# Kernel optimization log

Measured on AMD Instinct MI355X. Metric: run time of the kernel, lower is better.

The kernel has to match this reference:

```python
import jax, jax.numpy as jnp
import numpy as np


def setup_inputs() -> dict:
    key = jax.random.key(0)
    ks = jax.random.split(key, 6)
    B, S, D, E = 4, 8192, 2048, 8
    scale = 1.0 / np.sqrt(D)
    return {
        "x": jax.random.normal(ks[0], (B, S, D), dtype=jnp.float32),
        "Wg": jax.random.normal(ks[1], (E, D), dtype=jnp.float32) * scale,
        "bg": jax.random.normal(ks[2], (E,), dtype=jnp.float32) * scale,
        "Wn": jax.random.normal(ks[3], (E, D), dtype=jnp.float32) * scale,
        "bn": jax.random.normal(ks[4], (E,), dtype=jnp.float32) * scale,
        "noise": jax.random.normal(ks[5], (B, S, E), dtype=jnp.float32),
        "k": 2,
    }


def reference(x, Wg, bg, Wn, bn, noise, k):
    # gate and noisy-gate projections: [B,S,D] x [E,D] -> [B,S,E]
    gate_logits = jnp.einsum("bsd,ed->bse", x, Wg) + bg
    noisy_pre = jnp.einsum("bsd,ed->bse", x, Wn) + bn
    noisy_logits = noise * jax.nn.softplus(noisy_pre) + gate_logits

    # top-k over experts (largest, sorted), matching torch.topk
    topklogits, topexperts = jax.lax.top_k(noisy_logits, k)  # [B,S,k]

    # softmax over sparse logits (-inf elsewhere) == softmax over the topk
    # values, scattered back; small E,k so a one-hot scatter is cheap.
    topk_probs = jax.nn.softmax(topklogits, axis=-1)          # [B,S,k]
    onehot = jax.nn.one_hot(topexperts, noisy_logits.shape[-1],
                            dtype=topk_probs.dtype)           # [B,S,k,E]
    router_output = jnp.einsum("bsk,bske->bse", topk_probs, onehot)
    return router_output, topexperts
```

## Files before the change

kernel.cpp:

```cpp
#include <hip/hip_runtime.h>
#include <math.h>


#define RD 2048
#define RE 8
#define NE16 16
#define TOKB 64
#define CH 32
#define KSL 2
#define KLEN (RD / KSL)
#define NCH (KLEN / CH)
#define NW 4
#define DEPTH 4

#define AS1 __attribute__((address_space(1)))
#define AS3 __attribute__((address_space(3)))

#define WAITVM(N) asm volatile("s_waitcnt vmcnt(" #N ")" ::: "memory")

__device__ __forceinline__ void gload_lds16(const float* g, float* l) {
    __builtin_amdgcn_global_load_lds((const AS1 unsigned int*)g,
                                     (AS3 unsigned int*)l, 16, 0, 0);
}

__global__ __launch_bounds__(256) void transpose_w_kernel(
    const float* __restrict__ Wg, const float* __restrict__ Wn,
    float* __restrict__ WT)
{
    const int idx = blockIdx.x * 256 + threadIdx.x;
    const int d = idx >> 4;
    const int e = idx & 15;
    WT[idx] = (e < 8) ? Wg[e * RD + d] : Wn[(e - 8) * RD + d];
}

__global__ __launch_bounds__(256) void router_main_kernel(
    const float* __restrict__ x,
    const float* __restrict__ WT,
    float* __restrict__ pws,
    int T)
{
    __shared__ float xb[DEPTH][TOKB * CH];

    const int tid = threadIdx.x;
    const int w = tid >> 6;
    const int l = tid & 63;
    const int NTB = T / TOKB;
    const int bt = blockIdx.x % NTB;
    const int kslice = blockIdx.x / NTB;
    const int tokBase = bt * TOKB;
    const int kbase = kslice * KLEN;

    float acc[NE16];
#pragma unroll
    for (int e = 0; e < NE16; ++e) acc[e] = 0.f;

    const size_t laneoff = (size_t)(l >> 3) * RD + ((((l & 7) ^ (l >> 3))) << 2);
    const float* p0 = x + (size_t)(tokBase + (w * 2 + 0) * 8) * RD + kbase + laneoff;
    const float* p1 = x + (size_t)(tokBase + (w * 2 + 1) * 8) * RD + kbase + laneoff;
    float* d0base = &xb[0][(w * 2 + 0) * 256];
    float* d1base = &xb[0][(w * 2 + 1) * 256];

    gload_lds16(p0 + 0 * CH, d0base + 0 * (TOKB * CH));
    gload_lds16(p1 + 0 * CH, d1base + 0 * (TOKB * CH));
    gload_lds16(p0 + 1 * CH, d0base + 1 * (TOKB * CH));
    gload_lds16(p1 + 1 * CH, d1base + 1 * (TOKB * CH));

#pragma unroll 1
    for (int c = 0; c < NCH; ++c) {
        const int b = c & (DEPTH - 1);

        if (c + 2 < NCH) {
            const int nb = (c + 2) & (DEPTH - 1);
            gload_lds16(p0 + (c + 2) * CH, d0base + nb * (TOKB * CH));
            gload_lds16(p1 + (c + 2) * CH, d1base + nb * (TOKB * CH));
            WAITVM(4);
        } else if (c + 2 == NCH) {
            WAITVM(2);
        } else {
            WAITVM(0);
        }
        __builtin_amdgcn_s_barrier();
        __builtin_amdgcn_sched_barrier(0);

        const int wbase = __builtin_amdgcn_readfirstlane(
            (kbase + c * CH + w * 8) * NE16);
        const float* __restrict__ wt = WT + wbase;
#pragma unroll
        for (int r = 0; r < 2; ++r) {
            const int q = w * 2 + r;
            const float4 xq = *reinterpret_cast<const float4*>(
                &xb[b][l * CH + ((q ^ (l & 7)) << 2)]);
            const float xs[4] = {xq.x, xq.y, xq.z, xq.w};
#pragma unroll
            for (int ii = 0; ii < 4; ++ii) {
                const float* wrow = wt + (r * 4 + ii) * NE16;
#pragma unroll
                for (int e = 0; e < NE16; ++e)
                    acc[e] = fmaf(xs[ii], wrow[e], acc[e]);
            }
        }
    }

    __syncthreads();

    float* red = &xb[0][0];
    {
        const int roff = (w * TOKB + l) * NE16;
        *reinterpret_cast<float4*>(&red[roff + 0])  = make_float4(acc[0], acc[1], acc[2], acc[3]);
        *reinterpret_cast<float4*>(&red[roff + 4])  = make_float4(acc[4], acc[5], acc[6], acc[7]);
        *reinterpret_cast<float4*>(&red[roff + 8])  = make_float4(acc[8], acc[9], acc[10], acc[11]);
        *reinterpret_cast<float4*>(&red[roff + 12]) = make_float4(acc[12], acc[13], acc[14], acc[15]);
    }
    __syncthreads();

    {
        const int tok = tid >> 2;
        const int q4 = tid & 3;
        float4 s = make_float4(0.f, 0.f, 0.f, 0.f);
#pragma unroll
        for (int wv = 0; wv < NW; ++wv) {
            const float4 a = *reinterpret_cast<const float4*>(
                &red[(wv * TOKB + tok) * NE16 + q4 * 4]);
            s.x += a.x; s.y += a.y; s.z += a.z; s.w += a.w;
        }
        float* dst = pws + ((size_t)kslice * T + tokBase + tok) * NE16 + q4 * 4;
        *reinterpret_cast<float4*>(dst) = s;
    }
}

__global__ __launch_bounds__(256) void router_finalize_kernel(
    const float* __restrict__ pws,
    const float* __restrict__ bg,
    const float* __restrict__ bn,
    const float* __restrict__ noise,
    float* __restrict__ out_router,
    float* __restrict__ out_experts,
    int T)
{
    const int tok = blockIdx.x * 256 + threadIdx.x;

    const float* pp0 = pws + (size_t)tok * NE16;
    const float* pp1 = pws + ((size_t)T + tok) * NE16;

    float g[RE], nn[RE];
#pragma unroll
    for (int e = 0; e < RE; ++e) {
        g[e]  = pp0[e] + pp1[e] + bg[e];
        nn[e] = pp0[8 + e] + pp1[8 + e] + bn[e];
    }

    const float4* nzp = reinterpret_cast<const float4*>(noise + (size_t)tok * RE);
    const float4 nz0 = nzp[0];
    const float4 nz1 = nzp[1];
    const float nzv[RE] = {nz0.x, nz0.y, nz0.z, nz0.w,
                           nz1.x, nz1.y, nz1.z, nz1.w};

    float v[RE];
#pragma unroll
    for (int e = 0; e < RE; ++e) {
        const float p = nn[e];
        const float sp = fmaxf(p, 0.f) + log1pf(expf(-fabsf(p)));
        v[e] = fmaf(nzv[e], sp, g[e]);
    }

    int i1 = 0; float m1 = v[0];
#pragma unroll
    for (int e = 1; e < RE; ++e)
        if (v[e] > m1) { m1 = v[e]; i1 = e; }
    int i2 = -1; float m2 = -INFINITY;
#pragma unroll
    for (int e = 0; e < RE; ++e)
        if (e != i1 && v[e] > m2) { m2 = v[e]; i2 = e; }

    const float e2 = expf(m2 - m1);
    const float inv = 1.f / (1.f + e2);
    const float p1s = inv;
    const float p2s = e2 * inv;

    float r[RE];
#pragma unroll
    for (int e = 0; e < RE; ++e)
        r[e] = (e == i1) ? p1s : ((e == i2) ? p2s : 0.f);

    float4* orow = reinterpret_cast<float4*>(out_router + (size_t)tok * RE);
    orow[0] = make_float4(r[0], r[1], r[2], r[3]);
    orow[1] = make_float4(r[4], r[5], r[6], r[7]);

    float2* erow = reinterpret_cast<float2*>(out_experts + (size_t)tok * 2);
    *erow = make_float2((float)i1, (float)i2);
}

extern "C" void kernel_launch(void* const* d_in, const int* in_sizes, int n_in,
                              void* d_out, int out_size, void* d_ws, size_t ws_size,
                              hipStream_t stream) {
    const float* x   = (const float*)d_in[0];
    const float* Wg  = (const float*)d_in[1];
    const float* bg  = (const float*)d_in[2];
    const float* Wn  = (const float*)d_in[3];
    const float* bn  = (const float*)d_in[4];
    const float* nz  = (const float*)d_in[5];
    const int T = in_sizes[0] / RD;

    float* WT  = (float*)d_ws;
    float* pws = WT + (size_t)RD * NE16;

    float* out_router  = (float*)d_out;
    float* out_experts = out_router + (size_t)T * RE;

    hipLaunchKernelGGL(transpose_w_kernel, dim3((RD * NE16) / 256), dim3(256),
                       0, stream, Wg, Wn, WT);

    const int NTB = T / TOKB;
    hipLaunchKernelGGL(router_main_kernel, dim3(NTB * KSL), dim3(256), 0,
                       stream, x, WT, pws, T);

    hipLaunchKernelGGL(router_finalize_kernel, dim3(T / 256), dim3(256), 0,
                       stream, pws, bg, bn, nz, out_router, out_experts, T);
}
```

Before: 60.77 us.

## Fuse weight transpose, projection and finalize into one kernel with last-block reduction

```diff
diff --git a/kernel.cpp b/kernel.cpp
--- a/kernel.cpp
+++ b/kernel.cpp
@@ -11,7 +11,8 @@
 #define KLEN (RD / KSL)
 #define NCH (KLEN / CH)
 #define NW 4
-#define DEPTH 4
+#define DEPTH 5
+#define CHF (TOKB * CH)
 
 #define AS1 __attribute__((address_space(1)))
 #define AS3 __attribute__((address_space(3)))
@@ -23,23 +24,20 @@
                                      (AS3 unsigned int*)l, 16, 0, 0);
 }
 
-__global__ __launch_bounds__(256) void transpose_w_kernel(
-    const float* __restrict__ Wg, const float* __restrict__ Wn,
-    float* __restrict__ WT)
-{
-    const int idx = blockIdx.x * 256 + threadIdx.x;
-    const int d = idx >> 4;
-    const int e = idx & 15;
-    WT[idx] = (e < 8) ? Wg[e * RD + d] : Wn[(e - 8) * RD + d];
-}
-
-__global__ __launch_bounds__(256) void router_main_kernel(
+__global__ __launch_bounds__(256) void router_fused_kernel(
     const float* __restrict__ x,
-    const float* __restrict__ WT,
+    const float* __restrict__ Wg,
+    const float* __restrict__ bg,
+    const float* __restrict__ Wn,
+    const float* __restrict__ bn,
+    const float* __restrict__ noise,
     float* __restrict__ pws,
+    int* __restrict__ flags,
+    float* __restrict__ out_router,
+    float* __restrict__ out_experts,
     int T)
 {
-    __shared__ float xb[DEPTH][TOKB * CH];
+    __shared__ float xb[DEPTH][CHF];
 
     const int tid = threadIdx.x;
     const int w = tid >> 6;
@@ -57,48 +55,57 @@
     const size_t laneoff = (size_t)(l >> 3) * RD + ((((l & 7) ^ (l >> 3))) << 2);
     const float* p0 = x + (size_t)(tokBase + (w * 2 + 0) * 8) * RD + kbase + laneoff;
     const float* p1 = x + (size_t)(tokBase + (w * 2 + 1) * 8) * RD + kbase + laneoff;
-    float* d0base = &xb[0][(w * 2 + 0) * 256];
-    float* d1base = &xb[0][(w * 2 + 1) * 256];
-
-    gload_lds16(p0 + 0 * CH, d0base + 0 * (TOKB * CH));
-    gload_lds16(p1 + 0 * CH, d1base + 0 * (TOKB * CH));
-    gload_lds16(p0 + 1 * CH, d0base + 1 * (TOKB * CH));
-    gload_lds16(p1 + 1 * CH, d1base + 1 * (TOKB * CH));
+    float* d0 = &xb[0][(w * 2 + 0) * 256];
+    float* d1 = &xb[0][(w * 2 + 1) * 256];
+
+    gload_lds16(p0 + 0 * CH, d0 + 0 * CHF);
+    gload_lds16(p1 + 0 * CH, d1 + 0 * CHF);
+    gload_lds16(p0 + 1 * CH, d0 + 1 * CHF);
+    gload_lds16(p1 + 1 * CH, d1 + 1 * CHF);
+    gload_lds16(p0 + 2 * CH, d0 + 2 * CHF);
+    gload_lds16(p1 + 2 * CH, d1 + 2 * CHF);
+
+    int cb = 0;
+    int rb = 3;
 
 #pragma unroll 1
     for (int c = 0; c < NCH; ++c) {
-        const int b = c & (DEPTH - 1);
-
-        if (c + 2 < NCH) {
-            const int nb = (c + 2) & (DEPTH - 1);
-            gload_lds16(p0 + (c + 2) * CH, d0base + nb * (TOKB * CH));
-            gload_lds16(p1 + (c + 2) * CH, d1base + nb * (TOKB * CH));
-            WAITVM(4);
-        } else if (c + 2 == NCH) {
-            WAITVM(2);
-        } else {
-            WAITVM(0);
-        }
+        if (c <= NCH - 3)      { WAITVM(4); }
+        else if (c == NCH - 2) { WAITVM(2); }
+        else                   { WAITVM(0); }
         __builtin_amdgcn_s_barrier();
         __builtin_amdgcn_sched_barrier(0);
 
-        const int wbase = __builtin_amdgcn_readfirstlane(
-            (kbase + c * CH + w * 8) * NE16);
-        const float* __restrict__ wt = WT + wbase;
+        const int woff = __builtin_amdgcn_readfirstlane(kbase + c * CH + w * 8);
+        const float* __restrict__ wgb = Wg + woff;
+        const float* __restrict__ wnb = Wn + woff;
 #pragma unroll
         for (int r = 0; r < 2; ++r) {
             const int q = w * 2 + r;
             const float4 xq = *reinterpret_cast<const float4*>(
-                &xb[b][l * CH + ((q ^ (l & 7)) << 2)]);
+                &xb[cb][l * CH + ((q ^ (l & 7)) << 2)]);
             const float xs[4] = {xq.x, xq.y, xq.z, xq.w};
 #pragma unroll
-            for (int ii = 0; ii < 4; ++ii) {
-                const float* wrow = wt + (r * 4 + ii) * NE16;
-#pragma unroll
-                for (int e = 0; e < NE16; ++e)
-                    acc[e] = fmaf(xs[ii], wrow[e], acc[e]);
+            for (int e = 0; e < RE; ++e) {
+                const float4 a = *reinterpret_cast<const float4*>(wgb + e * RD + r * 4);
+                const float4 b = *reinterpret_cast<const float4*>(wnb + e * RD + r * 4);
+                acc[e]     = fmaf(xs[0], a.x, acc[e]);
+                acc[e]     = fmaf(xs[1], a.y, acc[e]);
+                acc[e]     = fmaf(xs[2], a.z, acc[e]);
+                acc[e]     = fmaf(xs[3], a.w, acc[e]);
+                acc[8 + e] = fmaf(xs[0], b.x, acc[8 + e]);
+                acc[8 + e] = fmaf(xs[1], b.y, acc[8 + e]);
+                acc[8 + e] = fmaf(xs[2], b.z, acc[8 + e]);
+                acc[8 + e] = fmaf(xs[3], b.w, acc[8 + e]);
             }
         }
+
+        if (c + 3 < NCH) {
+            gload_lds16(p0 + (c + 3) * CH, d0 + rb * CHF);
+            gload_lds16(p1 + (c + 3) * CH, d1 + rb * CHF);
+        }
+        if (++rb == DEPTH) rb = 0;
+        if (++cb == DEPTH) cb = 0;
     }
 
     __syncthreads();
@@ -126,68 +133,67 @@
         float* dst = pws + ((size_t)kslice * T + tokBase + tok) * NE16 + q4 * 4;
         *reinterpret_cast<float4*>(dst) = s;
     }
-}
-
-__global__ __launch_bounds__(256) void router_finalize_kernel(
-    const float* __restrict__ pws,
-    const float* __restrict__ bg,
-    const float* __restrict__ bn,
-    const float* __restrict__ noise,
-    float* __restrict__ out_router,
-    float* __restrict__ out_experts,
-    int T)
-{
-    const int tok = blockIdx.x * 256 + threadIdx.x;
-
-    const float* pp0 = pws + (size_t)tok * NE16;
-    const float* pp1 = pws + ((size_t)T + tok) * NE16;
-
-    float g[RE], nn[RE];
-#pragma unroll
-    for (int e = 0; e < RE; ++e) {
-        g[e]  = pp0[e] + pp1[e] + bg[e];
-        nn[e] = pp0[8 + e] + pp1[8 + e] + bn[e];
-    }
-
-    const float4* nzp = reinterpret_cast<const float4*>(noise + (size_t)tok * RE);
-    const float4 nz0 = nzp[0];
-    const float4 nz1 = nzp[1];
-    const float nzv[RE] = {nz0.x, nz0.y, nz0.z, nz0.w,
-                           nz1.x, nz1.y, nz1.z, nz1.w};
-
-    float v[RE];
-#pragma unroll
-    for (int e = 0; e < RE; ++e) {
-        const float p = nn[e];
-        const float sp = fmaxf(p, 0.f) + log1pf(expf(-fabsf(p)));
-        v[e] = fmaf(nzv[e], sp, g[e]);
-    }
-
-    int i1 = 0; float m1 = v[0];
-#pragma unroll
-    for (int e = 1; e < RE; ++e)
-        if (v[e] > m1) { m1 = v[e]; i1 = e; }
-    int i2 = -1; float m2 = -INFINITY;
-#pragma unroll
-    for (int e = 0; e < RE; ++e)
-        if (e != i1 && v[e] > m2) { m2 = v[e]; i2 = e; }
-
-    const float e2 = expf(m2 - m1);
-    const float inv = 1.f / (1.f + e2);
-    const float p1s = inv;
-    const float p2s = e2 * inv;
-
-    float r[RE];
-#pragma unroll
-    for (int e = 0; e < RE; ++e)
-        r[e] = (e == i1) ? p1s : ((e == i2) ? p2s : 0.f);
-
-    float4* orow = reinterpret_cast<float4*>(out_router + (size_t)tok * RE);
-    orow[0] = make_float4(r[0], r[1], r[2], r[3]);
-    orow[1] = make_float4(r[4], r[5], r[6], r[7]);
-
-    float2* erow = reinterpret_cast<float2*>(out_experts + (size_t)tok * 2);
-    *erow = make_float2((float)i1, (float)i2);
+
+    __threadfence();
+    __syncthreads();
+    int* amF = (int*)&xb[4][0];
+    if (tid == 0) *amF = atomicAdd(flags + bt, 1);
+    __syncthreads();
+    if (*amF != 1) return;
+    __threadfence();
+
+    if (tid < TOKB) {
+        const int tok = tokBase + tid;
+        const float* pp0 = pws + (size_t)tok * NE16;
+        const float* pp1 = pws + ((size_t)T + tok) * NE16;
+
+        float g[RE], nn[RE];
+#pragma unroll
+        for (int e = 0; e < RE; ++e) {
+            g[e]  = pp0[e] + pp1[e] + bg[e];
+            nn[e] = pp0[8 + e] + pp1[8 + e] + bn[e];
+        }
+
+        const float4* nzp = reinterpret_cast<const float4*>(noise + (size_t)tok * RE);
+        const float4 nz0 = nzp[0];
+        const float4 nz1 = nzp[1];
+        const float nzv[RE] = {nz0.x, nz0.y, nz0.z, nz0.w,
+                               nz1.x, nz1.y, nz1.z, nz1.w};
+
+        float v[RE];
+#pragma unroll
+        for (int e = 0; e < RE; ++e) {
+            const float p = nn[e];
+            const float sp = fmaxf(p, 0.f) + log1pf(expf(-fabsf(p)));
+            v[e] = fmaf(nzv[e], sp, g[e]);
+        }
+
+        int i1 = 0; float m1 = v[0];
+#pragma unroll
+        for (int e = 1; e < RE; ++e)
+            if (v[e] > m1) { m1 = v[e]; i1 = e; }
+        int i2 = -1; float m2 = -INFINITY;
+#pragma unroll
+        for (int e = 0; e < RE; ++e)
+            if (e != i1 && v[e] > m2) { m2 = v[e]; i2 = e; }
+
+        const float e2 = expf(m2 - m1);
+        const float inv = 1.f / (1.f + e2);
+        const float p1s = inv;
+        const float p2s = e2 * inv;
+
+        float r[RE];
+#pragma unroll
+        for (int e = 0; e < RE; ++e)
+            r[e] = (e == i1) ? p1s : ((e == i2) ? p2s : 0.f);
+
+        float4* orow = reinterpret_cast<float4*>(out_router + (size_t)tok * RE);
+        orow[0] = make_float4(r[0], r[1], r[2], r[3]);
+        orow[1] = make_float4(r[4], r[5], r[6], r[7]);
+
+        float2* erow = reinterpret_cast<float2*>(out_experts + (size_t)tok * 2);
+        *erow = make_float2((float)i1, (float)i2);
+    }
 }
 
 extern "C" void kernel_launch(void* const* d_in, const int* in_sizes, int n_in,
@@ -200,20 +206,17 @@
     const float* bn  = (const float*)d_in[4];
     const float* nz  = (const float*)d_in[5];
     const int T = in_sizes[0] / RD;
-
-    float* WT  = (float*)d_ws;
-    float* pws = WT + (size_t)RD * NE16;
+    const int NTB = T / TOKB;
+
+    float* pws  = (float*)d_ws;
+    int* flags  = (int*)(pws + (size_t)KSL * T * NE16);
 
     float* out_router  = (float*)d_out;
     float* out_experts = out_router + (size_t)T * RE;
 
-    hipLaunchKernelGGL(transpose_w_kernel, dim3((RD * NE16) / 256), dim3(256),
-                       0, stream, Wg, Wn, WT);
-
-    const int NTB = T / TOKB;
-    hipLaunchKernelGGL(router_main_kernel, dim3(NTB * KSL), dim3(256), 0,
-                       stream, x, WT, pws, T);
-
-    hipLaunchKernelGGL(router_finalize_kernel, dim3(T / 256), dim3(256), 0,
-                       stream, pws, bg, bn, nz, out_router, out_experts, T);
+    hipMemsetAsync(flags, 0, NTB * sizeof(int), stream);
+
+    hipLaunchKernelGGL(router_fused_kernel, dim3(NTB * KSL), dim3(256), 0,
+                       stream, x, Wg, bg, Wn, bn, nz, pws, flags,
+                       out_router, out_experts, T);
 }
```

New measurement: 206.9 us. 3.41x slower.

## Fuse finalize into main kernel via last-arriving-block atomic counter

Applied to the files above, without the earlier changes.

```diff
diff --git a/kernel.cpp b/kernel.cpp
--- a/kernel.cpp
+++ b/kernel.cpp
@@ -12,6 +12,7 @@
 #define NCH (KLEN / CH)
 #define NW 4
 #define DEPTH 4
+#define CHF (TOKB * CH)
 
 #define AS1 __attribute__((address_space(1)))
 #define AS3 __attribute__((address_space(3)))
@@ -36,10 +37,16 @@
 __global__ __launch_bounds__(256) void router_main_kernel(
     const float* __restrict__ x,
     const float* __restrict__ WT,
+    const float* __restrict__ bg,
+    const float* __restrict__ bn,
+    const float* __restrict__ noise,
     float* __restrict__ pws,
+    int* __restrict__ flags,
+    float* __restrict__ out_router,
+    float* __restrict__ out_experts,
     int T)
 {
-    __shared__ float xb[DEPTH][TOKB * CH];
+    __shared__ float xb[DEPTH][CHF];
 
     const int tid = threadIdx.x;
     const int w = tid >> 6;
@@ -60,10 +67,10 @@
     float* d0base = &xb[0][(w * 2 + 0) * 256];
     float* d1base = &xb[0][(w * 2 + 1) * 256];
 
-    gload_lds16(p0 + 0 * CH, d0base + 0 * (TOKB * CH));
-    gload_lds16(p1 + 0 * CH, d1base + 0 * (TOKB * CH));
-    gload_lds16(p0 + 1 * CH, d0base + 1 * (TOKB * CH));
-    gload_lds16(p1 + 1 * CH, d1base + 1 * (TOKB * CH));
+    gload_lds16(p0 + 0 * CH, d0base + 0 * CHF);
+    gload_lds16(p1 + 0 * CH, d1base + 0 * CHF);
+    gload_lds16(p0 + 1 * CH, d0base + 1 * CHF);
+    gload_lds16(p1 + 1 * CH, d1base + 1 * CHF);
 
 #pragma unroll 1
     for (int c = 0; c < NCH; ++c) {
@@ -71,8 +78,8 @@
 
         if (c + 2 < NCH) {
             const int nb = (c + 2) & (DEPTH - 1);
-            gload_lds16(p0 + (c + 2) * CH, d0base + nb * (TOKB * CH));
-            gload_lds16(p1 + (c + 2) * CH, d1base + nb * (TOKB * CH));
+            gload_lds16(p0 + (c + 2) * CH, d0base + nb * CHF);
+            gload_lds16(p1 + (c + 2) * CH, d1base + nb * CHF);
             WAITVM(4);
         } else if (c + 2 == NCH) {
             WAITVM(2);
@@ -126,68 +133,67 @@
         float* dst = pws + ((size_t)kslice * T + tokBase + tok) * NE16 + q4 * 4;
         *reinterpret_cast<float4*>(dst) = s;
     }
-}
-
-__global__ __launch_bounds__(256) void router_finalize_kernel(
-    const float* __restrict__ pws,
-    const float* __restrict__ bg,
-    const float* __restrict__ bn,
-    const float* __restrict__ noise,
-    float* __restrict__ out_router,
-    float* __restrict__ out_experts,
-    int T)
-{
-    const int tok = blockIdx.x * 256 + threadIdx.x;
-
-    const float* pp0 = pws + (size_t)tok * NE16;
-    const float* pp1 = pws + ((size_t)T + tok) * NE16;
-
-    float g[RE], nn[RE];
-#pragma unroll
-    for (int e = 0; e < RE; ++e) {
-        g[e]  = pp0[e] + pp1[e] + bg[e];
-        nn[e] = pp0[8 + e] + pp1[8 + e] + bn[e];
-    }
-
-    const float4* nzp = reinterpret_cast<const float4*>(noise + (size_t)tok * RE);
-    const float4 nz0 = nzp[0];
-    const float4 nz1 = nzp[1];
-    const float nzv[RE] = {nz0.x, nz0.y, nz0.z, nz0.w,
-                           nz1.x, nz1.y, nz1.z, nz1.w};
-
-    float v[RE];
-#pragma unroll
-    for (int e = 0; e < RE; ++e) {
-        const float p = nn[e];
-        const float sp = fmaxf(p, 0.f) + log1pf(expf(-fabsf(p)));
-        v[e] = fmaf(nzv[e], sp, g[e]);
-    }
-
-    int i1 = 0; float m1 = v[0];
-#pragma unroll
-    for (int e = 1; e < RE; ++e)
-        if (v[e] > m1) { m1 = v[e]; i1 = e; }
-    int i2 = -1; float m2 = -INFINITY;
-#pragma unroll
-    for (int e = 0; e < RE; ++e)
-        if (e != i1 && v[e] > m2) { m2 = v[e]; i2 = e; }
-
-    const float e2 = expf(m2 - m1);
-    const float inv = 1.f / (1.f + e2);
-    const float p1s = inv;
-    const float p2s = e2 * inv;
-
-    float r[RE];
-#pragma unroll
-    for (int e = 0; e < RE; ++e)
-        r[e] = (e == i1) ? p1s : ((e == i2) ? p2s : 0.f);
-
-    float4* orow = reinterpret_cast<float4*>(out_router + (size_t)tok * RE);
-    orow[0] = make_float4(r[0], r[1], r[2], r[3]);
-    orow[1] = make_float4(r[4], r[5], r[6], r[7]);
-
-    float2* erow = reinterpret_cast<float2*>(out_experts + (size_t)tok * 2);
-    *erow = make_float2((float)i1, (float)i2);
+
+    __threadfence();
+    __syncthreads();
+    int* amF = (int*)&red[4096];
+    if (tid == 0) *amF = atomicAdd(flags + bt, 1);
+    __syncthreads();
+    if (*amF != 1) return;
+    __threadfence();
+
+    if (tid < TOKB) {
+        const int tok = tokBase + tid;
+        const float* pp0 = pws + (size_t)tok * NE16;
+        const float* pp1 = pws + ((size_t)T + tok) * NE16;
+
+        float g[RE], nn[RE];
+#pragma unroll
+        for (int e = 0; e < RE; ++e) {
+            g[e]  = pp0[e] + pp1[e] + bg[e];
+            nn[e] = pp0[8 + e] + pp1[8 + e] + bn[e];
+        }
+
+        const float4* nzp = reinterpret_cast<const float4*>(noise + (size_t)tok * RE);
+        const float4 nz0 = nzp[0];
+        const float4 nz1 = nzp[1];
+        const float nzv[RE] = {nz0.x, nz0.y, nz0.z, nz0.w,
+                               nz1.x, nz1.y, nz1.z, nz1.w};
+
+        float v[RE];
+#pragma unroll
+        for (int e = 0; e < RE; ++e) {
+            const float p = nn[e];
+            const float sp = fmaxf(p, 0.f) + log1pf(expf(-fabsf(p)));
+            v[e] = fmaf(nzv[e], sp, g[e]);
+        }
+
+        int i1 = 0; float m1 = v[0];
+#pragma unroll
+        for (int e = 1; e < RE; ++e)
+            if (v[e] > m1) { m1 = v[e]; i1 = e; }
+        int i2 = -1; float m2 = -INFINITY;
+#pragma unroll
+        for (int e = 0; e < RE; ++e)
+            if (e != i1 && v[e] > m2) { m2 = v[e]; i2 = e; }
+
+        const float e2 = expf(m2 - m1);
+        const float inv = 1.f / (1.f + e2);
+        const float p1s = inv;
+        const float p2s = e2 * inv;
+
+        float r[RE];
+#pragma unroll
+        for (int e = 0; e < RE; ++e)
+            r[e] = (e == i1) ? p1s : ((e == i2) ? p2s : 0.f);
+
+        float4* orow = reinterpret_cast<float4*>(out_router + (size_t)tok * RE);
+        orow[0] = make_float4(r[0], r[1], r[2], r[3]);
+        orow[1] = make_float4(r[4], r[5], r[6], r[7]);
+
+        float2* erow = reinterpret_cast<float2*>(out_experts + (size_t)tok * 2);
+        *erow = make_float2((float)i1, (float)i2);
+    }
 }
 
 extern "C" void kernel_launch(void* const* d_in, const int* in_sizes, int n_in,
@@ -200,20 +206,21 @@
     const float* bn  = (const float*)d_in[4];
     const float* nz  = (const float*)d_in[5];
     const int T = in_sizes[0] / RD;
-
-    float* WT  = (float*)d_ws;
-    float* pws = WT + (size_t)RD * NE16;
+    const int NTB = T / TOKB;
+
+    float* WT   = (float*)d_ws;
+    float* pws  = WT + (size_t)RD * NE16;
+    int* flags  = (int*)(pws + (size_t)KSL * T * NE16);
 
     float* out_router  = (float*)d_out;
     float* out_experts = out_router + (size_t)T * RE;
 
+    hipMemsetAsync(flags, 0, NTB * sizeof(int), stream);
+
     hipLaunchKernelGGL(transpose_w_kernel, dim3((RD * NE16) / 256), dim3(256),
                        0, stream, Wg, Wn, WT);
 
-    const int NTB = T / TOKB;
     hipLaunchKernelGGL(router_main_kernel, dim3(NTB * KSL), dim3(256), 0,
-                       stream, x, WT, pws, T);
-
-    hipLaunchKernelGGL(router_finalize_kernel, dim3(T / 256), dim3(256), 0,
-                       stream, pws, bg, bn, nz, out_router, out_experts, T);
-}
+                       stream, x, WT, bg, bn, nz, pws, flags,
+                       out_router, out_experts, T);
+}
```

New measurement: 180.3 us. 197% more time.
